# Kernel optimization log

Measured on AMD Instinct MI355X. Metric: run time of the kernel, lower is better.

The kernel has to match this reference:

```python
import jax, jax.numpy as jnp
import numpy as np
import math

B, T, C, H = 2, 2048, 1024, 16
D = C // H  # head dim = 64

def setup_inputs() -> dict:
    key = jax.random.key(0)
    ks = jax.random.split(key, 9)
    s = 0.02
    return {
        "x": jax.random.normal(ks[0], (B, T, C), dtype=jnp.float32),
        "Wq": jax.random.normal(ks[1], (C, C), dtype=jnp.float32) * s,
        "bq": jax.random.normal(ks[2], (C,), dtype=jnp.float32) * s,
        "Wk": jax.random.normal(ks[3], (C, C), dtype=jnp.float32) * s,
        "bk": jax.random.normal(ks[4], (C,), dtype=jnp.float32) * s,
        "Wv": jax.random.normal(ks[5], (C, C), dtype=jnp.float32) * s,
        "bv": jax.random.normal(ks[6], (C,), dtype=jnp.float32) * s,
        "Wo": jax.random.normal(ks[7], (C, C), dtype=jnp.float32) * s,
        "bo": jax.random.normal(ks[8], (C,), dtype=jnp.float32) * s,
    }

def reference(x, Wq, bq, Wk, bk, Wv, bv, Wo, bo):
    # x: [B, T, C]; torch Linear is y = x @ W.T + b
    Bv_, Tv_, Cv_ = x.shape
    q = (x @ Wq.T + bq).reshape(Bv_, Tv_, H, D)
    k = (x @ Wk.T + bk).reshape(Bv_, Tv_, H, D)
    v = (x @ Wv.T + bv).reshape(Bv_, Tv_, H, D)
    scale = 1.0 / math.sqrt(D)
    # [B, H, Tq, Tk] attention scores
    att = jnp.einsum("bqhd,bkhd->bhqk", q, k) * scale
    causal = jnp.tril(jnp.ones((Tv_, Tv_), dtype=bool))  # [T, T]
    att = jnp.where(causal[None, None, :, :], att, -jnp.inf)
    att = jax.nn.softmax(att, axis=-1)
    y = jnp.einsum("bhqk,bkhd->bqhd", att, v).reshape(Bv_, Tv_, Cv_)
    return y @ Wo.T + bo
```

## Files before the change

kernel.cpp:

```cpp
#include <hip/hip_runtime.h>
#include <hip/hip_bf16.h>
#include <cstdint>
#include <cstddef>

typedef __attribute__((ext_vector_type(8))) short short8;
typedef __attribute__((ext_vector_type(4))) float f32x4;
typedef unsigned int u32;
typedef __attribute__((ext_vector_type(4))) u32 u32x4;

#define MFMA(a,b,c) __builtin_amdgcn_mfma_f32_16x16x32_bf16(a,b,c,0,0,0)

__device__ __forceinline__ void gload_lds16(const void* gptr, void* lptr) {
  __builtin_amdgcn_global_load_lds((const __attribute__((address_space(1))) u32*)gptr,
                                   (__attribute__((address_space(3))) u32*)lptr, 16, 0, 0);
}

template<int N> __device__ __forceinline__ void vm_wait() {
  asm volatile("s_waitcnt vmcnt(%0)" :: "n"(N) : "memory");
}

__device__ __forceinline__ void barrier_sync() {
  asm volatile("" ::: "memory");
  __builtin_amdgcn_s_barrier();
  asm volatile("" ::: "memory");
  __builtin_amdgcn_sched_barrier(0);
}

__device__ __forceinline__ unsigned short f2bf(float f) {
  __hip_bfloat16 h = __float2bfloat16(f);
  return *reinterpret_cast<unsigned short*>(&h);
}

__device__ __forceinline__ short8 ldg8(const unsigned short* p) {
  return *reinterpret_cast<const short8*>(p);
}

__device__ __forceinline__ u32 cvt_pk_bf16(float lo, float hi) {
  u32 r;
  asm("v_cvt_pk_bf16_f32 %0, %1, %2" : "=v"(r) : "v"(lo), "v"(hi));
  return r;
}

__global__ __launch_bounds__(256) void cvt_all_kernel(
    const float* __restrict__ x,
    const float* __restrict__ w0, const float* __restrict__ w1,
    const float* __restrict__ w2, const float* __restrict__ w3,
    unsigned short* __restrict__ xb,
    unsigned short* __restrict__ o0, unsigned short* __restrict__ o1,
    unsigned short* __restrict__ o2, unsigned short* __restrict__ o3)
{
  int id = blockIdx.x * blockDim.x + threadIdx.x;
  const float* in;
  unsigned short* out;
  int idx;
  if (id < 1048576) {
    in = x; out = xb; idx = id;
  } else {
    int r = id - 1048576;
    int z = r >> 18;
    idx = r & 262143;
    in  = (z == 0) ? w0 : (z == 1) ? w1 : (z == 2) ? w2 : w3;
    out = (z == 0) ? o0 : (z == 1) ? o1 : (z == 2) ? o2 : o3;
  }
  float4 f = reinterpret_cast<const float4*>(in)[idx];
  ushort4 o;
  o.x = f2bf(f.x); o.y = f2bf(f.y); o.z = f2bf(f.z); o.w = f2bf(f.w);
  reinterpret_cast<ushort4*>(out)[idx] = o;
}

template<int BM, int BN, int WM, int WN, bool F32OUT>
__device__ __forceinline__ void gemm2_body(
    const unsigned short* __restrict__ A,
    const unsigned short* __restrict__ W,
    const float* __restrict__ bias,
    unsigned short* __restrict__ outb, float* __restrict__ outf,
    int ldo, float oscale, int m0,
    unsigned short* __restrict__ outvt = nullptr, int n0g = 0)
{
  constexpr int K = 1024, BK = 32, NT = K / BK;
  constexpr int NTHR = WM * WN * 64;
  constexpr int FM = BM / (WM * 16);
  constexpr int FN = BN / (WN * 16);
  constexpr int NLA = BM * BK * 2 / (NTHR * 16);
  constexpr int NLB = BN * BK * 2 / (NTHR * 16);
  constexpr int NLD = NLA + NLB;

  __shared__ unsigned short As[3][BM * BK];
  __shared__ unsigned short Ws[3][BN * BK];

  const int tid = threadIdx.x;
  const int lane = tid & 63;
  const int wave = tid >> 6;
  const int wm = wave / WN, wn = wave % WN;
  const int wr = wm * FM * 16, wc = wn * FN * 16;
  const int lr = lane >> 4, lc = lane & 15;

  f32x4 acc[FM][FN] = {};

  const char* Ab = (const char*)(A + (size_t)m0 * K);
  const char* Wb = (const char*)W;

#define STAGE(buf, k0)                                                            \
  {                                                                               \
    _Pragma("unroll")                                                             \
    for (int i = 0; i < NLA; ++i) {                                               \
      int L = (i * NTHR + tid) * 16;                                              \
      int row = L >> 6;                                                           \
      int col = L & 63;                                                           \
      gload_lds16(Ab + (size_t)row * 2048 + (k0) * 2 + col, (char*)&As[buf][0] + L); \
    }                                                                             \
    _Pragma("unroll")                                                             \
    for (int i = 0; i < NLB; ++i) {                                               \
      int L = (i * NTHR + tid) * 16;                                              \
      int row = L >> 6;                                                           \
      int col = L & 63;                                                           \
      gload_lds16(Wb + (size_t)row * 2048 + (k0) * 2 + col, (char*)&Ws[buf][0] + L); \
    }                                                                             \
  }

#define COMPUTE(buf)                                                              \
  {                                                                               \
    short8 af[FM], bf[FN];                                                        \
    _Pragma("unroll")                                                             \
    for (int m = 0; m < FM; ++m) {                                                \
      int row = wr + m * 16 + lc;                                                 \
      af[m] = *reinterpret_cast<const short8*>(                                   \
          (const char*)&As[buf][0] + row * 64 + lr * 16);                         \
    }                                                                             \
    _Pragma("unroll")                                                             \
    for (int n = 0; n < FN; ++n) {                                                \
      int row = wc + n * 16 + lc;                                                 \
      bf[n] = *reinterpret_cast<const short8*>(                                   \
          (const char*)&Ws[buf][0] + row * 64 + lr * 16);                         \
    }                                                                             \
    __builtin_amdgcn_s_setprio(1);                                                \
    _Pragma("unroll")                                                             \
    for (int m = 0; m < FM; ++m)                                                  \
      _Pragma("unroll")                                                           \
      for (int n = 0; n < FN; ++n)                                                \
        acc[m][n] = MFMA(af[m], bf[n], acc[m][n]);                                \
    __builtin_amdgcn_s_setprio(0);                                                \
  }

  STAGE(0, 0)
  STAGE(1, BK)
  int cur = 0, stg = 2;
#pragma unroll 1
  for (int kt = 0; kt < NT; ++kt) {
    if (kt < NT - 1) { vm_wait<NLD>(); }
    else            { vm_wait<0>();   }
    barrier_sync();
    COMPUTE(cur)
    if (kt + 2 < NT) STAGE(stg, (kt + 2) * BK)
    cur = (cur == 2) ? 0 : cur + 1;
    stg = (stg == 2) ? 0 : stg + 1;
  }

#undef STAGE
#undef COMPUTE

  if (!F32OUT && outvt != nullptr) {
#pragma unroll
    for (int m = 0; m < FM; ++m)
#pragma unroll
      for (int n = 0; n < FN; ++n)
#pragma unroll
        for (int r = 0; r < 4; ++r) {
          int row = m0 + wr + m * 16 + lr * 4 + r;
          int gcol = n0g + wc + n * 16 + lc;
          float v = (acc[m][n][r] + bias[wc + n * 16 + lc]) * oscale;
          int bb = row >> 11, tt = row & 2047;
          outvt[(size_t)(bb * 1024 + gcol) * 2048 + tt] = f2bf(v);
        }
    return;
  }

#pragma unroll
  for (int m = 0; m < FM; ++m)
#pragma unroll
    for (int n = 0; n < FN; ++n)
#pragma unroll
      for (int r = 0; r < 4; ++r) {
        int row = m0 + wr + m * 16 + lr * 4 + r;
        int col = wc + n * 16 + lc;
        float v = (acc[m][n][r] + bias[col]) * oscale;
        if (F32OUT) outf[(size_t)row * ldo + col] = v;
        else        outb[(size_t)row * ldo + col] = f2bf(v);
      }
}

__global__ __launch_bounds__(256, 3) void gemm_qkv5(
    const unsigned short* __restrict__ xb,
    const unsigned short* __restrict__ Wqb, const unsigned short* __restrict__ Wkb,
    const unsigned short* __restrict__ Wvb,
    const float* __restrict__ bq, const float* __restrict__ bk, const float* __restrict__ bv,
    unsigned short* __restrict__ Q, unsigned short* __restrict__ Ko,
    unsigned short* __restrict__ VT)
{
  const int i = blockIdx.x;
  const int sw = (i & 7) * 96 + (i >> 3);
  const int z  = sw >> 8;
  const int rr = sw & 255;
  const int m0 = (rr >> 3) * 128;
  const int nr = (rr & 7) * 128;
  const unsigned short* W = ((z == 0) ? Wqb : (z == 1) ? Wkb : Wvb) + (size_t)nr * 1024;
  const float* bias = ((z == 0) ? bq : (z == 1) ? bk : bv) + nr;
  const float oscale = (z == 0) ? 0.18033688011112042f : 1.0f;
  if (z == 2) {
    gemm2_body<128, 128, 2, 2, false>(xb, W, bias, nullptr, nullptr, 1024, oscale, m0, VT, nr);
  } else {
    unsigned short* out = ((z == 0) ? Q : Ko) + nr;
    gemm2_body<128, 128, 2, 2, false>(xb, W, bias, out, nullptr, 1024, oscale, m0);
  }
}

__global__ __launch_bounds__(256, 2) void gemm_out3(
    const unsigned short* __restrict__ Y, const unsigned short* __restrict__ Wob,
    const float* __restrict__ bo, float* __restrict__ out)
{
  const int i = blockIdx.x;
  const int sw = (i & 7) * 64 + (i >> 3);
  const int by = sw >> 3;
  const int bx = sw & 7;
  const int m0 = by * 64;
  const int n0 = bx * 128;
  gemm2_body<64, 128, 2, 2, true>(Y, Wob + (size_t)n0 * 1024, bo + n0, nullptr, out + n0,
                                  1024, 1.0f, m0);
}

__global__ __launch_bounds__(256) void attn_kernel(
    const unsigned short* __restrict__ Q, const unsigned short* __restrict__ K,
    const unsigned short* __restrict__ VT, unsigned short* __restrict__ Y)
{
  __shared__ unsigned short Ks[2][64 * 64];
  __shared__ unsigned short Vs[2][64 * 64];
  __shared__ u32 Pl[4][512];

  const int i   = blockIdx.x;
  const int xcd = i & 7;
  const int j   = i >> 3;
  const int bh  = xcd + 8 * (j & 3);
  const int qb  = 31 - (j >> 2);
  const int b = bh >> 4, h = bh & 15;
  const int tid = threadIdx.x;
  const int wave = tid >> 6;
  const int lane = tid & 63;
  const int lr = lane >> 4;
  const int lc = lane & 15;
  const float M = 4.0f;

  const unsigned short* Kbh = K + (size_t)b * 2048 * 1024 + h * 64;
  const unsigned short* Vbh = VT + (size_t)bh * 64 * 2048;
  u32* pw = Pl[wave];
  const int psw = (lc & 7) << 2;

  u32 ov = 0x3F803F80u;
  u32x4 ones4 = {ov, ov, ov, ov};
  short8 ones = *reinterpret_cast<short8*>(&ones4);

  const int q0 = qb * 64 + wave * 16;
  const unsigned short* qp = &Q[((size_t)(b * 2048 + q0 + lc)) * 1024 + h * 64 + lr * 8];
  short8 qa0 = ldg8(qp);
  short8 qa1 = ldg8(qp + 32);

  f32x4 o[4] = {};
  f32x4 lacc = {};

  const int nt = qb + 1;
  int cur = 0;

#pragma unroll
  for (int ii = 0; ii < 2; ++ii) {
    int L = (ii * 256 + tid) * 16;
    int row = L >> 7;
    int src = (L & 127) ^ ((row & 7) << 4);
    gload_lds16((const char*)(Kbh + (size_t)row * 1024) + src, (char*)&Ks[0][0] + L);
    gload_lds16((const char*)(Vbh + (size_t)row * 2048) + src, (char*)&Vs[0][0] + L);
  }
  __syncthreads();

  for (int t = 0; t < nt; ++t) {
    if (t + 1 < nt) {
      const int tk1 = (t + 1) * 64;
#pragma unroll
      for (int ii = 0; ii < 2; ++ii) {
        int L = (ii * 256 + tid) * 16;
        int row = L >> 7;
        int src = (L & 127) ^ ((row & 7) << 4);
        gload_lds16((const char*)(Kbh + (size_t)(tk1 + row) * 1024) + src, (char*)&Ks[cur ^ 1][0] + L);
        gload_lds16((const char*)(Vbh + (size_t)row * 2048 + tk1) + src, (char*)&Vs[cur ^ 1][0] + L);
      }
    }

    const int tk0 = t * 64;
    const unsigned short* Kt = Ks[cur];
    const unsigned short* Vt = Vs[cur];

    f32x4 s[4] = {};
#pragma unroll
    for (int kt = 0; kt < 4; ++kt) {
      int row = kt * 16 + lc;
      int sw = (row & 7) << 4;
      short8 kb0 = *reinterpret_cast<const short8*>((const char*)Kt + row * 128 + ((lr * 16) ^ sw));
      short8 kb1 = *reinterpret_cast<const short8*>((const char*)Kt + row * 128 + ((64 + lr * 16) ^ sw));
      __builtin_amdgcn_s_setprio(1);
      s[kt] = MFMA(kb0, qa0, s[kt]);
      s[kt] = MFMA(kb1, qa1, s[kt]);
      __builtin_amdgcn_s_setprio(0);
    }

    const bool diag = (t == qb);
    float p[4][4];
#pragma unroll
    for (int kt = 0; kt < 4; ++kt)
#pragma unroll
      for (int r = 0; r < 4; ++r)
        p[kt][r] = __builtin_amdgcn_exp2f(s[kt][r] - M);
    if (diag) {
#pragma unroll
      for (int kt = 0; kt < 4; ++kt)
#pragma unroll
        for (int r = 0; r < 4; ++r)
          if (tk0 + kt * 16 + lr * 4 + r > q0 + lc) p[kt][r] = 0.f;
    }

#pragma unroll
    for (int kt = 0; kt < 4; ++kt) {
      uint2 w;
      w.x = cvt_pk_bf16(p[kt][0], p[kt][1]);
      w.y = cvt_pk_bf16(p[kt][2], p[kt][3]);
      *reinterpret_cast<uint2*>(&pw[lc * 32 + ((kt * 8 + lr * 2) ^ psw)]) = w;
    }
    short8 pa0 = *reinterpret_cast<const short8*>(&pw[lc * 32 + ((lr * 4) ^ psw)]);
    short8 pa1 = *reinterpret_cast<const short8*>(&pw[lc * 32 + ((16 + lr * 4) ^ psw)]);

    __builtin_amdgcn_s_setprio(1);
    lacc = MFMA(pa0, ones, lacc);
    lacc = MFMA(pa1, ones, lacc);
    __builtin_amdgcn_s_setprio(0);

#pragma unroll
    for (int ntt = 0; ntt < 4; ++ntt) {
      int row = ntt * 16 + lc;
      int sw = (row & 7) << 4;
      short8 v0 = *reinterpret_cast<const short8*>((const char*)Vt + row * 128 + ((lr * 16) ^ sw));
      short8 v1 = *reinterpret_cast<const short8*>((const char*)Vt + row * 128 + ((64 + lr * 16) ^ sw));
      __builtin_amdgcn_s_setprio(1);
      o[ntt] = MFMA(pa0, v0, o[ntt]);
      o[ntt] = MFMA(pa1, v1, o[ntt]);
      __builtin_amdgcn_s_setprio(0);
    }

    __syncthreads();
    cur ^= 1;
  }

  float rl[4];
#pragma unroll
  for (int r = 0; r < 4; ++r) rl[r] = __builtin_amdgcn_rcpf(lacc[r]);
#pragma unroll
  for (int ntt = 0; ntt < 4; ++ntt)
#pragma unroll
    for (int r = 0; r < 4; ++r) {
      float val = o[ntt][r] * rl[r];
      int row = b * 2048 + q0 + lr * 4 + r;
      Y[(size_t)row * 1024 + h * 64 + ntt * 16 + lc] = f2bf(val);
    }
}

extern "C" void kernel_launch(void* const* d_in, const int* in_sizes, int n_in,
                              void* d_out, int out_size, void* d_ws, size_t ws_size,
                              hipStream_t stream)
{
  const float* x  = (const float*)d_in[0];
  const float* Wq = (const float*)d_in[1];
  const float* bq = (const float*)d_in[2];
  const float* Wk = (const float*)d_in[3];
  const float* bk = (const float*)d_in[4];
  const float* Wv = (const float*)d_in[5];
  const float* bv = (const float*)d_in[6];
  const float* Wo = (const float*)d_in[7];
  const float* bo = (const float*)d_in[8];
  float* out = (float*)d_out;

  char* ws = (char*)d_ws;
  unsigned short* xb  = (unsigned short*)(ws);
  unsigned short* Wqb = (unsigned short*)(ws + 8388608);
  unsigned short* Wkb = (unsigned short*)(ws + 8388608 + 2097152);
  unsigned short* Wvb = (unsigned short*)(ws + 8388608 + 2 * 2097152);
  unsigned short* Wob = (unsigned short*)(ws + 8388608 + 3 * 2097152);
  unsigned short* Qb  = (unsigned short*)(ws + 16777216);
  unsigned short* Kb  = (unsigned short*)(ws + 16777216 + 8388608);
  unsigned short* VTb = (unsigned short*)(ws + 16777216 + 3 * 8388608);
  unsigned short* Yb  = (unsigned short*)(ws + 16777216 + 4 * 8388608);

  cvt_all_kernel<<<8192, 256, 0, stream>>>(x, Wq, Wk, Wv, Wo, xb, Wqb, Wkb, Wvb, Wob);

  gemm_qkv5<<<768, 256, 0, stream>>>(xb, Wqb, Wkb, Wvb, bq, bk, bv, Qb, Kb, VTb);
  attn_kernel<<<1024, 256, 0, stream>>>(Qb, Kb, VTb, Yb);
  gemm_out3<<<512, 256, 0, stream>>>(Yb, Wob, bo, out);
}
```

Baseline: 103.6 us.

## Pair early and late causal query tiles per attention block to share K/V loads

Each attention block now processes two query tiles (q-block p and 31-p) for the same head, iterating over K/V tiles once and applying the second tile's compute only while its causal range is active. This balances per-block causal work and halves the K/V global-to-LDS traffic per query tile. The grid shrinks from 1024 to 512 blocks, and the doubled accumulators raise register pressure, which could reduce occupancy or latency hiding.

Measured after the change: 107.7 us. +3.9%, slower.

```diff
diff --git a/kernel.cpp b/kernel.cpp
--- a/kernel.cpp
+++ b/kernel.cpp
@@ -238,9 +238,10 @@
 
   const int i   = blockIdx.x;
   const int xcd = i & 7;
-  const int j   = i >> 3;
-  const int bh  = xcd + 8 * (j & 3);
-  const int qb  = 31 - (j >> 2);
+  const int bh  = xcd + 8 * ((i >> 3) & 3);
+  const int p   = i >> 5;
+  const int qA  = 31 - p;
+  const int qB  = p;
   const int b = bh >> 4, h = bh & 15;
   const int tid = threadIdx.x;
   const int wave = tid >> 6;
@@ -258,16 +259,72 @@
   u32x4 ones4 = {ov, ov, ov, ov};
   short8 ones = *reinterpret_cast<short8*>(&ones4);
 
-  const int q0 = qb * 64 + wave * 16;
-  const unsigned short* qp = &Q[((size_t)(b * 2048 + q0 + lc)) * 1024 + h * 64 + lr * 8];
-  short8 qa0 = ldg8(qp);
-  short8 qa1 = ldg8(qp + 32);
-
-  f32x4 o[4] = {};
-  f32x4 lacc = {};
-
-  const int nt = qb + 1;
+  const int q0A = qA * 64 + wave * 16;
+  const int q0B = qB * 64 + wave * 16;
+  const unsigned short* qpA = &Q[((size_t)(b * 2048 + q0A + lc)) * 1024 + h * 64 + lr * 8];
+  const unsigned short* qpB = &Q[((size_t)(b * 2048 + q0B + lc)) * 1024 + h * 64 + lr * 8];
+  short8 qaA0 = ldg8(qpA), qaA1 = ldg8(qpA + 32);
+  short8 qaB0 = ldg8(qpB), qaB1 = ldg8(qpB + 32);
+
+  f32x4 oA[4] = {}, oB[4] = {};
+  f32x4 laccA = {}, laccB = {};
+
+  const int nt = qA + 1;
   int cur = 0;
+
+#define ATT_COMPUTE(QF0, QF1, OO, LL, Q0, QT)                                     \
+  {                                                                               \
+    f32x4 s[4] = {};                                                              \
+    _Pragma("unroll")                                                             \
+    for (int kt = 0; kt < 4; ++kt) {                                              \
+      int row = kt * 16 + lc;                                                     \
+      int sw = (row & 7) << 4;                                                    \
+      short8 kb0 = *reinterpret_cast<const short8*>((const char*)Kt + row * 128 + ((lr * 16) ^ sw)); \
+      short8 kb1 = *reinterpret_cast<const short8*>((const char*)Kt + row * 128 + ((64 + lr * 16) ^ sw)); \
+      __builtin_amdgcn_s_setprio(1);                                              \
+      s[kt] = MFMA(kb0, QF0, s[kt]);                                              \
+      s[kt] = MFMA(kb1, QF1, s[kt]);                                              \
+      __builtin_amdgcn_s_setprio(0);                                              \
+    }                                                                             \
+    const bool diag = (t == (QT));                                                \
+    float pr[4][4];                                                               \
+    _Pragma("unroll")                                                             \
+    for (int kt = 0; kt < 4; ++kt)                                                \
+      _Pragma("unroll")                                                           \
+      for (int r = 0; r < 4; ++r)                                                 \
+        pr[kt][r] = __builtin_amdgcn_exp2f(s[kt][r] - M);                         \
+    if (diag) {                                                                   \
+      _Pragma("unroll")                                                           \
+      for (int kt = 0; kt < 4; ++kt)                                              \
+        _Pragma("unroll")                                                         \
+        for (int r = 0; r < 4; ++r)                                               \
+          if (tk0 + kt * 16 + lr * 4 + r > (Q0) + lc) pr[kt][r] = 0.f;            \
+    }                                                                             \
+    _Pragma("unroll")                                                             \
+    for (int kt = 0; kt < 4; ++kt) {                                              \
+      uint2 w;                                                                    \
+      w.x = cvt_pk_bf16(pr[kt][0], pr[kt][1]);                                    \
+      w.y = cvt_pk_bf16(pr[kt][2], pr[kt][3]);                                    \
+      *reinterpret_cast<uint2*>(&pw[lc * 32 + ((kt * 8 + lr * 2) ^ psw)]) = w;    \
+    }                                                                             \
+    short8 pa0 = *reinterpret_cast<const short8*>(&pw[lc * 32 + ((lr * 4) ^ psw)]); \
+    short8 pa1 = *reinterpret_cast<const short8*>(&pw[lc * 32 + ((16 + lr * 4) ^ psw)]); \
+    __builtin_amdgcn_s_setprio(1);                                                \
+    LL = MFMA(pa0, ones, LL);                                                     \
+    LL = MFMA(pa1, ones, LL);                                                     \
+    __builtin_amdgcn_s_setprio(0);                                                \
+    _Pragma("unroll")                                                             \
+    for (int ntt = 0; ntt < 4; ++ntt) {                                           \
+      int row = ntt * 16 + lc;                                                    \
+      int sw = (row & 7) << 4;                                                    \
+      short8 v0 = *reinterpret_cast<const short8*>((const char*)Vt + row * 128 + ((lr * 16) ^ sw)); \
+      short8 v1 = *reinterpret_cast<const short8*>((const char*)Vt + row * 128 + ((64 + lr * 16) ^ sw)); \
+      __builtin_amdgcn_s_setprio(1);                                              \
+      OO[ntt] = MFMA(pa0, v0, OO[ntt]);                                           \
+      OO[ntt] = MFMA(pa1, v1, OO[ntt]);                                           \
+      __builtin_amdgcn_s_setprio(0);                                              \
+    }                                                                             \
+  }
 
 #pragma unroll
   for (int ii = 0; ii < 2; ++ii) {
@@ -279,6 +336,7 @@
   }
   __syncthreads();
 
+#pragma unroll 1
   for (int t = 0; t < nt; ++t) {
     if (t + 1 < nt) {
       const int tk1 = (t + 1) * 64;
@@ -296,75 +354,31 @@
     const unsigned short* Kt = Ks[cur];
     const unsigned short* Vt = Vs[cur];
 
-    f32x4 s[4] = {};
-#pragma unroll
-    for (int kt = 0; kt < 4; ++kt) {
-      int row = kt * 16 + lc;
-      int sw = (row & 7) << 4;
-      short8 kb0 = *reinterpret_cast<const short8*>((const char*)Kt + row * 128 + ((lr * 16) ^ sw));
-      short8 kb1 = *reinterpret_cast<const short8*>((const char*)Kt + row * 128 + ((64 + lr * 16) ^ sw));
-      __builtin_amdgcn_s_setprio(1);
-      s[kt] = MFMA(kb0, qa0, s[kt]);
-      s[kt] = MFMA(kb1, qa1, s[kt]);
-      __builtin_amdgcn_s_setprio(0);
-    }
-
-    const bool diag = (t == qb);
-    float p[4][4];
-#pragma unroll
-    for (int kt = 0; kt < 4; ++kt)
-#pragma unroll
-      for (int r = 0; r < 4; ++r)
-        p[kt][r] = __builtin_amdgcn_exp2f(s[kt][r] - M);
-    if (diag) {
-#pragma unroll
-      for (int kt = 0; kt < 4; ++kt)
-#pragma unroll
-        for (int r = 0; r < 4; ++r)
-          if (tk0 + kt * 16 + lr * 4 + r > q0 + lc) p[kt][r] = 0.f;
-    }
-
-#pragma unroll
-    for (int kt = 0; kt < 4; ++kt) {
-      uint2 w;
-      w.x = cvt_pk_bf16(p[kt][0], p[kt][1]);
-      w.y = cvt_pk_bf16(p[kt][2], p[kt][3]);
-      *reinterpret_cast<uint2*>(&pw[lc * 32 + ((kt * 8 + lr * 2) ^ psw)]) = w;
-    }
-    short8 pa0 = *reinterpret_cast<const short8*>(&pw[lc * 32 + ((lr * 4) ^ psw)]);
-    short8 pa1 = *reinterpret_cast<const short8*>(&pw[lc * 32 + ((16 + lr * 4) ^ psw)]);
-
-    __builtin_amdgcn_s_setprio(1);
-    lacc = MFMA(pa0, ones, lacc);
-    lacc = MFMA(pa1, ones, lacc);
-    __builtin_amdgcn_s_setprio(0);
-
-#pragma unroll
-    for (int ntt = 0; ntt < 4; ++ntt) {
-      int row = ntt * 16 + lc;
-      int sw = (row & 7) << 4;
-      short8 v0 = *reinterpret_cast<const short8*>((const char*)Vt + row * 128 + ((lr * 16) ^ sw));
-      short8 v1 = *reinterpret_cast<const short8*>((const char*)Vt + row * 128 + ((64 + lr * 16) ^ sw));
-      __builtin_amdgcn_s_setprio(1);
-      o[ntt] = MFMA(pa0, v0, o[ntt]);
-      o[ntt] = MFMA(pa1, v1, o[ntt]);
-      __builtin_amdgcn_s_setprio(0);
+    ATT_COMPUTE(qaA0, qaA1, oA, laccA, q0A, qA)
+    if (t <= qB) {
+      ATT_COMPUTE(qaB0, qaB1, oB, laccB, q0B, qB)
     }
 
     __syncthreads();
     cur ^= 1;
   }
 
-  float rl[4];
-#pragma unroll
-  for (int r = 0; r < 4; ++r) rl[r] = __builtin_amdgcn_rcpf(lacc[r]);
+#undef ATT_COMPUTE
+
+  float rlA[4], rlB[4];
+#pragma unroll
+  for (int r = 0; r < 4; ++r) {
+    rlA[r] = __builtin_amdgcn_rcpf(laccA[r]);
+    rlB[r] = __builtin_amdgcn_rcpf(laccB[r]);
+  }
 #pragma unroll
   for (int ntt = 0; ntt < 4; ++ntt)
 #pragma unroll
     for (int r = 0; r < 4; ++r) {
-      float val = o[ntt][r] * rl[r];
-      int row = b * 2048 + q0 + lr * 4 + r;
-      Y[(size_t)row * 1024 + h * 64 + ntt * 16 + lc] = f2bf(val);
+      int rowA = b * 2048 + q0A + lr * 4 + r;
+      Y[(size_t)rowA * 1024 + h * 64 + ntt * 16 + lc] = f2bf(oA[ntt][r] * rlA[r]);
+      int rowB = b * 2048 + q0B + lr * 4 + r;
+      Y[(size_t)rowB * 1024 + h * 64 + ntt * 16 + lc] = f2bf(oB[ntt][r] * rlB[r]);
     }
 }
 
@@ -397,6 +411,6 @@
   cvt_all_kernel<<<8192, 256, 0, stream>>>(x, Wq, Wk, Wv, Wo, xb, Wqb, Wkb, Wvb, Wob);
 
   gemm_qkv5<<<768, 256, 0, stream>>>(xb, Wqb, Wkb, Wvb, bq, bk, bv, Qb, Kb, VTb);
-  attn_kernel<<<1024, 256, 0, stream>>>(Qb, Kb, VTb, Yb);
+  attn_kernel<<<512, 256, 0, stream>>>(Qb, Kb, VTb, Yb);
   gemm_out3<<<512, 256, 0, stream>>>(Yb, Wob, bo, out);
 }
```
